# Kernel optimization log

Hardware: AMD Instinct MI355X
Metric: run time of the kernel (lower is better)

The kernel has to match this reference:

```python
import jax, jax.numpy as jnp
import numpy as np

E = 8        # num_experts
D_IN = 512   # num_inputs
H = 256      # num_neurons_expert
T = 64       # num_neurons_tower
B = 16384    # batch


def setup_inputs() -> dict:
    key = jax.random.key(0)
    ks = jax.random.split(key, 7)
    s_in = 1.0 / np.sqrt(D_IN)
    s_h = 1.0 / np.sqrt(H)
    return {
        "xv": jax.random.normal(ks[0], (B, D_IN), dtype=jnp.float32),
        # expert weights stacked: torch Linear weight is (out,in) -> (E, H, D_IN)
        "We": jax.random.uniform(ks[1], (E, H, D_IN), jnp.float32, -s_in, s_in),
        "be": jax.random.uniform(ks[2], (E, H), jnp.float32, -s_in, s_in),
        "Wg": jax.random.uniform(ks[3], (E, D_IN), jnp.float32, -s_in, s_in),
        "bg": jax.random.uniform(ks[4], (E,), jnp.float32, -s_in, s_in),
        "Wt": jax.random.uniform(ks[5], (T, H), jnp.float32, -s_h, s_h),
        "bt": jax.random.uniform(ks[6], (T,), jnp.float32, -s_h, s_h),
    }


def reference(xv, We, be, Wg, bg, Wt, bt):
    # All experts as one batched GEMM: [B,D] x [E,H,D] -> [B,E,H]
    experts = jax.nn.relu(jnp.einsum("bd,ehd->beh", xv, We) + be[None, :, :])
    # Dropout is identity in eval mode.
    gate = jax.nn.softmax(xv @ Wg.T + bg, axis=1)            # [B,E]
    combined = jnp.einsum("beh,be->bh", experts, gate)        # [B,H]
    out = jax.nn.sigmoid(combined @ Wt.T + bt)                # [B,T]
    return out
```

## Files before the change

kernel.cpp:

```cpp
#include <hip/hip_runtime.h>
#include <hip/hip_bf16.h>
#include <stdint.h>

typedef unsigned short u16;
typedef __bf16 bf16x8 __attribute__((ext_vector_type(8)));
typedef float f32x4 __attribute__((ext_vector_type(4)));

#define LDS_B_OFF 32768

__device__ __forceinline__ void glds16(const void* g, void* l) {
  __builtin_amdgcn_global_load_lds(
      (const __attribute__((address_space(1))) unsigned int*)g,
      (__attribute__((address_space(3))) unsigned int*)l, 16, 0, 0);
}

__device__ __forceinline__ u16 f2bf(float f) {
  unsigned int u = __builtin_bit_cast(unsigned int, f);
  u += 0x7fffu + ((u >> 16) & 1u);
  return (u16)(u >> 16);
}

__global__ __launch_bounds__(256) void prep_kernel(
    const float* __restrict__ xv, const float* __restrict__ We,
    const float* __restrict__ Wg, const float* __restrict__ bg,
    const float* __restrict__ Wt,
    u16* __restrict__ xv_bf, u16* __restrict__ We_bf,
    u16* __restrict__ Wt_bf, float* __restrict__ gate) {
  const int bx = blockIdx.x;
  if (bx < 4096) {
    const int wid = threadIdx.x >> 6, lane = threadIdx.x & 63;
    const int row = bx * 4 + wid;
    const float* xr = xv + (row << 9) + lane * 8;
    float4 x0 = *(const float4*)xr;
    float4 x1 = *(const float4*)(xr + 4);
    uint4 o;
    o.x = (unsigned)f2bf(x0.x) | ((unsigned)f2bf(x0.y) << 16);
    o.y = (unsigned)f2bf(x0.z) | ((unsigned)f2bf(x0.w) << 16);
    o.z = (unsigned)f2bf(x1.x) | ((unsigned)f2bf(x1.y) << 16);
    o.w = (unsigned)f2bf(x1.z) | ((unsigned)f2bf(x1.w) << 16);
    *(uint4*)(xv_bf + (row << 9) + lane * 8) = o;
    float s[8];
#pragma unroll
    for (int e = 0; e < 8; e++) {
      const float* wg = Wg + (e << 9) + lane * 8;
      float4 w0 = *(const float4*)wg;
      float4 w1 = *(const float4*)(wg + 4);
      s[e] = x0.x * w0.x + x0.y * w0.y + x0.z * w0.z + x0.w * w0.w +
             x1.x * w1.x + x1.y * w1.y + x1.z * w1.z + x1.w * w1.w;
    }
#pragma unroll
    for (int e = 0; e < 8; e++) {
#pragma unroll
      for (int off = 32; off > 0; off >>= 1) s[e] += __shfl_xor(s[e], off);
      s[e] += bg[e];
    }
    float mx = s[0];
#pragma unroll
    for (int e = 1; e < 8; e++) mx = fmaxf(mx, s[e]);
    float p[8], sum = 0.f;
#pragma unroll
    for (int e = 0; e < 8; e++) { p[e] = __expf(s[e] - mx); sum += p[e]; }
    float inv = 1.f / sum;
    if (lane == 0) {
      float4 g0 = {p[0] * inv, p[1] * inv, p[2] * inv, p[3] * inv};
      float4 g1 = {p[4] * inv, p[5] * inv, p[6] * inv, p[7] * inv};
      *(float4*)(gate + row * 8) = g0;
      *(float4*)(gate + row * 8 + 4) = g1;
    }
  } else {
    const int base = (bx - 4096) * 2048 + threadIdx.x * 8;
    const float* src;
    u16* dst;
    if (base < 1048576) { src = We + base; dst = We_bf + base; }
    else { src = Wt + (base - 1048576); dst = Wt_bf + (base - 1048576); }
    float4 a = *(const float4*)src;
    float4 b = *(const float4*)(src + 4);
    uint4 o;
    o.x = (unsigned)f2bf(a.x) | ((unsigned)f2bf(a.y) << 16);
    o.y = (unsigned)f2bf(a.z) | ((unsigned)f2bf(a.w) << 16);
    o.z = (unsigned)f2bf(b.x) | ((unsigned)f2bf(b.y) << 16);
    o.w = (unsigned)f2bf(b.z) | ((unsigned)f2bf(b.w) << 16);
    *(uint4*)dst = o;
  }
}

__global__ __launch_bounds__(256, 2) void moe_main(
    const u16* __restrict__ xv_bf, const u16* __restrict__ We_bf,
    const float* __restrict__ be, const float* __restrict__ gate,
    const u16* __restrict__ Wt_bf, float* __restrict__ part) {
  __shared__ u16 lds[40960];

  const int bx = ((blockIdx.x & 7) << 6) | (blockIdx.x >> 3);
  const int mb = bx >> 1;
  const int hb = bx & 1;
  const int m0 = mb << 6;
  const int tid = threadIdx.x;
  const int lane = tid & 63;
  const int wid = tid >> 6;
  const int wm = wid >> 1;
  const int wn = wid & 1;
  const int l15 = lane & 15;
  const int l4 = lane >> 4;

#pragma unroll
  for (int r = 0; r < 16; r++) {
    int gi = r * 256 + tid;
    int m = gi >> 6, s = gi & 63;
    int g = (s & ~7) | ((s & 7) ^ (m & 7));
    glds16(xv_bf + ((m0 + m) << 9) + (g << 3), &lds[gi << 3]);
  }

  f32x4 comb[2][4];
#pragma unroll
  for (int mt = 0; mt < 2; mt++)
#pragma unroll
    for (int nt = 0; nt < 4; nt++) comb[mt][nt] = {0.f, 0.f, 0.f, 0.f};

  for (int e = 0; e < 8; e++) {
    f32x4 acc[2][4];
#pragma unroll
    for (int mt = 0; mt < 2; mt++)
#pragma unroll
      for (int nt = 0; nt < 4; nt++) acc[mt][nt] = {0.f, 0.f, 0.f, 0.f};

    const u16* Wb = We_bf + (e << 17) + (hb << 16);
    for (int kc = 0; kc < 8; kc++) {
      __syncthreads();
#pragma unroll
      for (int r = 0; r < 4; r++) {
        int gi = r * 256 + tid;
        int n = gi >> 3, s = gi & 7;
        int g = s ^ (n & 7);
        glds16(Wb + (n << 9) + (kc << 6) + (g << 3), &lds[LDS_B_OFF + (gi << 3)]);
      }
      __syncthreads();
#pragma unroll
      for (int ks = 0; ks < 2; ks++) {
        bf16x8 af[2], bfr[4];
#pragma unroll
        for (int mt = 0; mt < 2; mt++) {
          int row = wm * 32 + mt * 16 + l15;
          int gk = kc * 8 + ks * 4 + l4;
          int slot = (gk & ~7) | ((gk & 7) ^ (row & 7));
          af[mt] = *(const bf16x8*)&lds[(row << 9) + (slot << 3)];
        }
#pragma unroll
        for (int nt = 0; nt < 4; nt++) {
          int n = wn * 64 + nt * 16 + l15;
          int gB = ks * 4 + l4;
          int slot = gB ^ (n & 7);
          bfr[nt] = *(const bf16x8*)&lds[LDS_B_OFF + (n << 6) + (slot << 3)];
        }
#pragma unroll
        for (int mt = 0; mt < 2; mt++)
#pragma unroll
          for (int nt = 0; nt < 4; nt++)
            acc[mt][nt] = __builtin_amdgcn_mfma_f32_16x16x32_bf16(
                af[mt], bfr[nt], acc[mt][nt], 0, 0, 0);
      }
    }
    float bev[4];
#pragma unroll
    for (int nt = 0; nt < 4; nt++)
      bev[nt] = be[(e << 8) + (hb << 7) + wn * 64 + nt * 16 + l15];
#pragma unroll
    for (int mt = 0; mt < 2; mt++) {
#pragma unroll
      for (int i = 0; i < 4; i++) {
        float g = gate[((m0 + wm * 32 + mt * 16 + l4 * 4 + i) << 3) + e];
#pragma unroll
        for (int nt = 0; nt < 4; nt++)
          comb[mt][nt][i] += g * fmaxf(acc[mt][nt][i] + bev[nt], 0.f);
      }
    }
  }

  __syncthreads();
#pragma unroll
  for (int mt = 0; mt < 2; mt++)
#pragma unroll
    for (int i = 0; i < 4; i++) {
      int row = wm * 32 + mt * 16 + l4 * 4 + i;
#pragma unroll
      for (int nt = 0; nt < 4; nt++) {
        int col = wn * 64 + nt * 16 + l15;
        __bf16 v = (__bf16)comb[mt][nt][i];
        lds[row * 136 + col] = __builtin_bit_cast(u16, v);
      }
    }
  __syncthreads();
  f32x4 tacc[4];
#pragma unroll
  for (int nt = 0; nt < 4; nt++) tacc[nt] = {0.f, 0.f, 0.f, 0.f};
  const u16* WtB = Wt_bf + (hb << 7);
#pragma unroll
  for (int kc = 0; kc < 4; kc++) {
    int ko = kc * 32 + l4 * 8;
    bf16x8 aT = *(const bf16x8*)&lds[(wid * 16 + l15) * 136 + ko];
#pragma unroll
    for (int nt = 0; nt < 4; nt++) {
      bf16x8 bT = *(const bf16x8*)&WtB[(nt * 16 + l15) * 256 + ko];
      tacc[nt] = __builtin_amdgcn_mfma_f32_16x16x32_bf16(aT, bT, tacc[nt], 0, 0, 0);
    }
  }
  float* pout = part + hb * 1048576;
#pragma unroll
  for (int nt = 0; nt < 4; nt++)
#pragma unroll
    for (int i = 0; i < 4; i++) {
      int grow = m0 + wid * 16 + l4 * 4 + i;
      pout[grow * 64 + nt * 16 + l15] = tacc[nt][i];
    }
}

__global__ __launch_bounds__(256) void finish_kernel(
    const float* __restrict__ part, const float* __restrict__ bt,
    float* __restrict__ out) {
  const int idx = (blockIdx.x * 256 + threadIdx.x) << 2;
  float4 a = *(const float4*)(part + idx);
  float4 b = *(const float4*)(part + 1048576 + idx);
  float4 c = *(const float4*)(bt + (idx & 63));
  float4 r;
  r.x = 1.f / (1.f + __expf(-(a.x + b.x + c.x)));
  r.y = 1.f / (1.f + __expf(-(a.y + b.y + c.y)));
  r.z = 1.f / (1.f + __expf(-(a.z + b.z + c.z)));
  r.w = 1.f / (1.f + __expf(-(a.w + b.w + c.w)));
  *(float4*)(out + idx) = r;
}

extern "C" void kernel_launch(void* const* d_in, const int* in_sizes, int n_in,
                              void* d_out, int out_size, void* d_ws, size_t ws_size,
                              hipStream_t stream) {
  const float* xv = (const float*)d_in[0];
  const float* We = (const float*)d_in[1];
  const float* be = (const float*)d_in[2];
  const float* Wg = (const float*)d_in[3];
  const float* bg = (const float*)d_in[4];
  const float* Wt = (const float*)d_in[5];
  const float* bt = (const float*)d_in[6];

  char* ws = (char*)d_ws;
  u16* xv_bf = (u16*)ws;
  u16* We_bf = (u16*)(ws + 16777216);
  u16* Wt_bf = (u16*)(ws + 18874368);
  float* gate = (float*)(ws + 18907136);
  float* part = (float*)(ws + 19431424);

  prep_kernel<<<4616, 256, 0, stream>>>(xv, We, Wg, bg, Wt, xv_bf, We_bf, Wt_bf, gate);
  moe_main<<<512, 256, 0, stream>>>(xv_bf, We_bf, be, gate, Wt_bf, part);
  finish_kernel<<<1024, 256, 0, stream>>>(part, bt, (float*)d_out);
}
```

Measured before the change: 147.1 us.

## Double-buffer expert weight tiles in LDS with one-step-ahead prefetch

The expert-weight K loop moves from 64-wide chunks with a load/sync/compute pattern to 32-wide chunks flattened across all experts. The next chunk is issued into an alternate LDS buffer before computing on the current one, so there is one barrier per step instead of two. The aim is to overlap global-to-LDS weight loads with MFMA work and cut barrier stalls. Smaller chunks mean more iterations and barriers overall. The barrier's implicit memory wait may still serialise on the prefetch, which limits the overlap.

```diff
diff --git a/kernel.cpp b/kernel.cpp
--- a/kernel.cpp
+++ b/kernel.cpp
@@ -109,6 +109,17 @@
     int g = (s & ~7) | ((s & 7) ^ (m & 7));
     glds16(xv_bf + ((m0 + m) << 9) + (g << 3), &lds[gi << 3]);
   }
+  {
+    const u16* Wb0 = We_bf + (hb << 16);
+#pragma unroll
+    for (int r = 0; r < 2; r++) {
+      int gi = r * 256 + tid;
+      int n = gi >> 2, s = gi & 3;
+      int g = s ^ (n & 3);
+      glds16(Wb0 + (n << 9) + (g << 3), &lds[LDS_B_OFF + (gi << 3)]);
+    }
+  }
+  __syncthreads();
 
   f32x4 comb[2][4];
 #pragma unroll
@@ -123,41 +134,43 @@
 #pragma unroll
       for (int nt = 0; nt < 4; nt++) acc[mt][nt] = {0.f, 0.f, 0.f, 0.f};
 
-    const u16* Wb = We_bf + (e << 17) + (hb << 16);
-    for (int kc = 0; kc < 8; kc++) {
+#pragma unroll
+    for (int kk = 0; kk < 16; kk++) {
+      const int t = e * 16 + kk;
+      if (t < 127) {
+        const int tn = t + 1;
+        const u16* Wbn = We_bf + ((tn >> 4) << 17) + (hb << 16) + ((tn & 15) << 5);
+#pragma unroll
+        for (int r = 0; r < 2; r++) {
+          int gi = r * 256 + tid;
+          int n = gi >> 2, s = gi & 3;
+          int g = s ^ (n & 3);
+          glds16(Wbn + (n << 9) + (g << 3),
+                 &lds[LDS_B_OFF + ((tn & 1) << 12) + (gi << 3)]);
+        }
+      }
+      const u16* Bb = &lds[LDS_B_OFF + ((t & 1) << 12)];
+      bf16x8 af[2], bfr[4];
+#pragma unroll
+      for (int mt = 0; mt < 2; mt++) {
+        int row = wm * 32 + mt * 16 + l15;
+        int gA = kk * 4 + l4;
+        int slot = (gA & ~7) | ((gA & 7) ^ (row & 7));
+        af[mt] = *(const bf16x8*)&lds[(row << 9) + (slot << 3)];
+      }
+#pragma unroll
+      for (int nt = 0; nt < 4; nt++) {
+        int n = wn * 64 + nt * 16 + l15;
+        int slot = l4 ^ (n & 3);
+        bfr[nt] = *(const bf16x8*)&Bb[(n << 5) + (slot << 3)];
+      }
+#pragma unroll
+      for (int mt = 0; mt < 2; mt++)
+#pragma unroll
+        for (int nt = 0; nt < 4; nt++)
+          acc[mt][nt] = __builtin_amdgcn_mfma_f32_16x16x32_bf16(
+              af[mt], bfr[nt], acc[mt][nt], 0, 0, 0);
       __syncthreads();
-#pragma unroll
-      for (int r = 0; r < 4; r++) {
-        int gi = r * 256 + tid;
-        int n = gi >> 3, s = gi & 7;
-        int g = s ^ (n & 7);
-        glds16(Wb + (n << 9) + (kc << 6) + (g << 3), &lds[LDS_B_OFF + (gi << 3)]);
-      }
-      __syncthreads();
-#pragma unroll
-      for (int ks = 0; ks < 2; ks++) {
-        bf16x8 af[2], bfr[4];
-#pragma unroll
-        for (int mt = 0; mt < 2; mt++) {
-          int row = wm * 32 + mt * 16 + l15;
-          int gk = kc * 8 + ks * 4 + l4;
-          int slot = (gk & ~7) | ((gk & 7) ^ (row & 7));
-          af[mt] = *(const bf16x8*)&lds[(row << 9) + (slot << 3)];
-        }
-#pragma unroll
-        for (int nt = 0; nt < 4; nt++) {
-          int n = wn * 64 + nt * 16 + l15;
-          int gB = ks * 4 + l4;
-          int slot = gB ^ (n & 7);
-          bfr[nt] = *(const bf16x8*)&lds[LDS_B_OFF + (n << 6) + (slot << 3)];
-        }
-#pragma unroll
-        for (int mt = 0; mt < 2; mt++)
-#pragma unroll
-          for (int nt = 0; nt < 4; nt++)
-            acc[mt][nt] = __builtin_amdgcn_mfma_f32_16x16x32_bf16(
-                af[mt], bfr[nt], acc[mt][nt], 0, 0, 0);
-      }
     }
     float bev[4];
 #pragma unroll
```

Result: faster. 142.9 us (-2.8%).
